# Performance work log

Measured on AMD Instinct MI355X. Metric: run time of the kernel, lower is better.

Reference implementation:

```python
import jax, jax.numpy as jnp
import numpy as np

NF, NLOC, NNEI = 4, 2048, 64
EMBED, PAIR_DIM, H = 128, 64, 8
HD = EMBED // H
EPS = 1e-5

def _ln(x, g, b):
    m = x.mean(-1, keepdims=True)
    v = ((x - m) ** 2).mean(-1, keepdims=True)
    return (x - m) * jax.lax.rsqrt(v + EPS) * g + b

def setup_inputs() -> dict:
    key = jax.random.key(0)
    ks = jax.random.split(key, 12)
    inp = {
        "query": jax.random.normal(ks[0], (NF, NLOC, EMBED), jnp.float32),
        "pair": jax.random.normal(ks[1], (NF, NLOC, NNEI, PAIR_DIM), jnp.float32),
        "nlist": jax.random.randint(ks[2], (NF, NLOC, NNEI), 0, NLOC, jnp.int64),
        "delta_pos": jax.random.normal(ks[3], (NF, NLOC, NNEI, 3), jnp.float32),
        "attn_mask": jnp.zeros((NF, H, NLOC, NNEI), jnp.float32),
        "ln_g": jnp.ones((EMBED,), jnp.float32),
        "ln_b": jnp.zeros((EMBED,), jnp.float32),
        "pn_g": jnp.ones((PAIR_DIM,), jnp.float32),
        "pn_b": jnp.zeros((PAIR_DIM,), jnp.float32),
        "Wq": jax.random.normal(ks[4], (EMBED, EMBED), jnp.float32) * (EMBED ** -0.5),
        "Wk": jax.random.normal(ks[5], (EMBED, EMBED), jnp.float32) * (EMBED ** -0.5),
        "Wv": jax.random.normal(ks[6], (EMBED, EMBED), jnp.float32) * (EMBED ** -0.5),
        "Wbias": jax.random.normal(ks[7], (H, PAIR_DIM), jnp.float32) * (PAIR_DIM ** -0.5),
        "bbias": jnp.zeros((H,), jnp.float32),
        "Wforce": jax.random.normal(ks[8], (1, EMBED), jnp.float32) * (EMBED ** -0.5),
    }
    return inp

def reference(query, pair, nlist, delta_pos, attn_mask,
              ln_g, ln_b, pn_g, pn_b, Wq, Wk, Wv, Wbias, bbias, Wforce):
    nf, nloc, _ = query.shape
    nnei = nlist.shape[-1]
    qn = _ln(query, ln_g, ln_b)            # [f,l,e]
    pn = _ln(pair, pn_g, pn_b)             # [f,l,n,p]
    scaling = HD ** -0.5
    q = (qn @ Wq.T).reshape(nf, nloc, H, HD) * scaling       # [f,l,h,d]
    k = qn @ Wk.T                                            # [f,l,e]
    v = qn @ Wv.T
    idx = nlist.reshape(nf, -1)[..., None]                   # [f,l*n,1]
    kg = jnp.take_along_axis(k, idx, axis=1).reshape(nf, nloc, nnei, H, HD)
    vg = jnp.take_along_axis(v, idx, axis=1).reshape(nf, nloc, nnei, H, HD)
    attn = jnp.einsum('flhd,flnhd->fhln', q, kg)             # [f,h,l,n]
    bias = jnp.einsum('flnp,hp->fhln', pn, Wbias) + bbias[None, :, None, None]
    probs = jax.nn.softmax(attn + attn_mask + bias, axis=-1)  # dropout off (eval)
    # rotate by delta_pos and contract with v over neighbors
    x = jnp.einsum('fhln,flnc,flnhd->flchd', probs, delta_pos, vg)
    x = x.reshape(nf, nloc, 3, EMBED)
    force = (x @ Wforce.T).squeeze(-1)                       # [f,l,3]
    return force
```

## Files before the change

kernel.cpp:

```cpp
#include <hip/hip_runtime.h>

#define NFR   4
#define NLOCC 2048
#define NNEIN 64
#define EMB   128
#define PDIM  64
#define NH    8
#define LNEPS 1e-5f
#define NROW  (NFR*NLOCC)

#define WS_Q   0
#define WS_K   (NROW*EMB)
#define WS_FV  (2*NROW*EMB)
#define WS_WVF (2*NROW*EMB + NROW*NH)
#define WS_G   (WS_WVF + NH*EMB)
#define WS_SG  (WS_G + NH*PDIM)

__device__ __forceinline__ void fma4(float4& acc, const float4 a, const float4 b) {
    acc.x = fmaf(a.x, b.x, acc.x);
    acc.y = fmaf(a.y, b.y, acc.y);
    acc.z = fmaf(a.z, b.z, acc.z);
    acc.w = fmaf(a.w, b.w, acc.w);
}
__device__ __forceinline__ void fma4s(float4& acc, const float s, const float4 b) {
    acc.x = fmaf(s, b.x, acc.x);
    acc.y = fmaf(s, b.y, acc.y);
    acc.z = fmaf(s, b.z, acc.z);
    acc.w = fmaf(s, b.w, acc.w);
}
__device__ __forceinline__ float hsum4(const float4 a) {
    return (a.x + a.y) + (a.z + a.w);
}
__device__ __forceinline__ float4 scale4(const float4 a, const float s) {
    return make_float4(a.x*s, a.y*s, a.z*s, a.w*s);
}

__global__ __launch_bounds__(256) void precompute_kernel(
    const float* __restrict__ pn_g, const float* __restrict__ pn_b,
    const float* __restrict__ Wbias, const float* __restrict__ bbias,
    const float* __restrict__ Wv, const float* __restrict__ Wforce,
    float* __restrict__ ws)
{
    const int t = threadIdx.x;
    {
        const int h  = t >> 5;
        const int e0 = (t & 31) * 4;
        float4 acc = make_float4(0.f, 0.f, 0.f, 0.f);
        #pragma unroll
        for (int d = 0; d < 16; ++d) {
            const float wf = Wforce[h*16 + d];
            const float4 wv = *(const float4*)(Wv + (size_t)(h*16 + d)*EMB + e0);
            fma4s(acc, wf, wv);
        }
        *(float4*)(ws + WS_WVF + (size_t)h*EMB + e0) = acc;
    }
    for (int idx = t; idx < NH*PDIM; idx += 256) {
        const int h = idx >> 6, p = idx & 63;
        ws[WS_G + idx] = pn_g[p] * Wbias[h*PDIM + p];
    }
    if (t < NH) {
        float sg = 0.f, c = 0.f;
        #pragma unroll 8
        for (int p = 0; p < PDIM; ++p) {
            const float wb = Wbias[t*PDIM + p];
            sg = fmaf(pn_g[p], wb, sg);
            c  = fmaf(pn_b[p], wb, c);
        }
        ws[WS_SG + t]      = sg;
        ws[WS_SG + NH + t] = c + bbias[t];
    }
}

__global__ __launch_bounds__(256, 2) void qkfv_kernel(
    const float* __restrict__ query,
    const float* __restrict__ ln_g, const float* __restrict__ ln_b,
    const float* __restrict__ Wq, const float* __restrict__ Wk,
    float* __restrict__ ws)
{
    __shared__ float gb_s[2][EMB];
    __shared__ float qn_s[16*132];
    __shared__ float wt_s[2][16*132];
    const int t = threadIdx.x;
    const int rowbase = blockIdx.x * 16;

    if (t < 64) {
        const float* src = (t < 32) ? ln_g : ln_b;
        ((float4*)gb_s[t >> 5])[t & 31] = ((const float4*)src)[t & 31];
    }

    const int r   = t >> 4;
    const int seg = t & 15;
    float4 x0 = ((const float4*)query)[(size_t)(rowbase + r)*32 + seg*2 + 0];
    float4 x1 = ((const float4*)query)[(size_t)(rowbase + r)*32 + seg*2 + 1];
    float s  = (x0.x + x0.y) + (x0.z + x0.w) + (x1.x + x1.y) + (x1.z + x1.w);
    float ss = x0.x*x0.x + x0.y*x0.y + x0.z*x0.z + x0.w*x0.w
             + x1.x*x1.x + x1.y*x1.y + x1.z*x1.z + x1.w*x1.w;
    #pragma unroll
    for (int m = 1; m < 16; m <<= 1) {
        s  += __shfl_xor(s,  m, 64);
        ss += __shfl_xor(ss, m, 64);
    }
    const float mean = s * (1.0f / 128.0f);
    const float var  = ss * (1.0f / 128.0f) - mean * mean;
    const float rstd = rsqrtf(var + LNEPS);
    __syncthreads();

    {
        const int c0 = seg * 8;
        float4 o0, o1;
        o0.x = (x0.x - mean)*rstd*gb_s[0][c0+0] + gb_s[1][c0+0];
        o0.y = (x0.y - mean)*rstd*gb_s[0][c0+1] + gb_s[1][c0+1];
        o0.z = (x0.z - mean)*rstd*gb_s[0][c0+2] + gb_s[1][c0+2];
        o0.w = (x0.w - mean)*rstd*gb_s[0][c0+3] + gb_s[1][c0+3];
        o1.x = (x1.x - mean)*rstd*gb_s[0][c0+4] + gb_s[1][c0+4];
        o1.y = (x1.y - mean)*rstd*gb_s[0][c0+5] + gb_s[1][c0+5];
        o1.z = (x1.z - mean)*rstd*gb_s[0][c0+6] + gb_s[1][c0+6];
        o1.w = (x1.w - mean)*rstd*gb_s[0][c0+7] + gb_s[1][c0+7];
        ((float4*)qn_s)[r*33 + seg*2 + 0] = o0;
        ((float4*)qn_s)[r*33 + seg*2 + 1] = o1;
    }
    __syncthreads();

    const int rp = t >> 5;
    const int r0 = rp * 2;
    const int cq = t & 31;
    const int sc0 = t >> 2;
    const int si0 = t & 3;
    const float4* qn4 = (const float4*)qn_s;

    for (int w = 0; w < 2; ++w) {
        const float4* W4 = (const float4*)((w == 0) ? Wq : Wk);
        float4 acc0 = make_float4(0.f,0.f,0.f,0.f);
        float4 acc1 = make_float4(0.f,0.f,0.f,0.f);
        {
            float4 g0 = W4[(size_t)sc0*32 + si0];
            float4 g1 = W4[(size_t)(sc0+64)*32 + si0];
            float* wt = wt_s[0];
            wt[(si0*4+0)*132 + sc0] = g0.x; wt[(si0*4+1)*132 + sc0] = g0.y;
            wt[(si0*4+2)*132 + sc0] = g0.z; wt[(si0*4+3)*132 + sc0] = g0.w;
            wt[(si0*4+0)*132 + sc0+64] = g1.x; wt[(si0*4+1)*132 + sc0+64] = g1.y;
            wt[(si0*4+2)*132 + sc0+64] = g1.z; wt[(si0*4+3)*132 + sc0+64] = g1.w;
        }
        __syncthreads();
        #pragma unroll
        for (int tau = 0; tau < 8; ++tau) {
            const int buf = tau & 1;
            float4 ng0, ng1;
            if (tau < 7) {
                ng0 = W4[(size_t)sc0*32 + (tau+1)*4 + si0];
                ng1 = W4[(size_t)(sc0+64)*32 + (tau+1)*4 + si0];
            }
            const float4* wt4 = (const float4*)wt_s[buf];
            #pragma unroll
            for (int e4 = 0; e4 < 4; ++e4) {
                float4 a0 = qn4[r0*33 + tau*4 + e4];
                float4 a1 = qn4[(r0+1)*33 + tau*4 + e4];
                const float* a0p = (const float*)&a0;
                const float* a1p = (const float*)&a1;
                #pragma unroll
                for (int ee = 0; ee < 4; ++ee) {
                    const float4 wv = wt4[(e4*4+ee)*33 + cq];
                    fma4s(acc0, a0p[ee], wv);
                    fma4s(acc1, a1p[ee], wv);
                }
            }
            if (tau < 7) {
                float* wt = wt_s[buf ^ 1];
                wt[(si0*4+0)*132 + sc0] = ng0.x; wt[(si0*4+1)*132 + sc0] = ng0.y;
                wt[(si0*4+2)*132 + sc0] = ng0.z; wt[(si0*4+3)*132 + sc0] = ng0.w;
                wt[(si0*4+0)*132 + sc0+64] = ng1.x; wt[(si0*4+1)*132 + sc0+64] = ng1.y;
                wt[(si0*4+2)*132 + sc0+64] = ng1.z; wt[(si0*4+3)*132 + sc0+64] = ng1.w;
            }
            __syncthreads();
        }
        const float sc = (w == 0) ? 0.25f : 1.0f;
        float4* dst = (float4*)(ws + (w == 0 ? WS_Q : WS_K));
        dst[(size_t)(rowbase + r0)*32 + cq]     = scale4(acc0, sc);
        dst[(size_t)(rowbase + r0 + 1)*32 + cq] = scale4(acc1, sc);
    }

    if (t < 128) {
        const int rr = t >> 3, h = t & 7;
        const float4* wvf4 = (const float4*)(ws + WS_WVF + (size_t)h*EMB);
        float4 acc = make_float4(0.f,0.f,0.f,0.f);
        #pragma unroll
        for (int ch = 0; ch < 32; ++ch)
            fma4(acc, qn4[rr*33 + ch], wvf4[ch]);
        ws[WS_FV + (size_t)(rowbase + rr)*NH + h] = hsum4(acc);
    }
}

__global__ __launch_bounds__(256, 4) void attn_force_kernel(
    const float* __restrict__ pair, const int* __restrict__ nlist,
    const float* __restrict__ delta_pos, const float* __restrict__ attn_mask,
    const float* __restrict__ ws, float* __restrict__ out)
{
    __shared__ float4 lds_k4[4*16*33];
    __shared__ float4 q_s4[32];
    __shared__ float4 G_s4[128];
    __shared__ float  csg_s[16];
    __shared__ float  logit_s[NNEIN*9];
    __shared__ float  s_s[NNEIN];
    __shared__ int    nl_s[NNEIN];

    const int t = threadIdx.x;
    const int bid = blockIdx.x;
    const int fr = bid >> 11;
    const int l  = bid & 2047;

    if (t < 16) ((int4*)nl_s)[t] = ((const int4*)(nlist + (size_t)bid*NNEIN))[t];
    __syncthreads();

    {
        const int w = t >> 6, lane = t & 63;
        const int half = lane >> 5, c = lane & 31;
        const float4* k4 = (const float4*)(ws + WS_K);
        int jj[8];
        #pragma unroll
        for (int i = 0; i < 8; ++i)
            jj[i] = nl_s[(w << 4) | (i << 1) | half];
        float4 vv[8];
        #pragma unroll
        for (int i = 0; i < 8; ++i)
            vv[i] = k4[((size_t)(fr << 11) + jj[i])*32 + c];
        #pragma unroll
        for (int i = 0; i < 8; ++i)
            lds_k4[(w*16 + ((i << 1) | half))*33 + c] = vv[i];
    }
    if (t < 32)        q_s4[t]      = ((const float4*)(ws + WS_Q + (size_t)bid*EMB))[t];
    else if (t < 160)  G_s4[t - 32] = ((const float4*)(ws + WS_G))[t - 32];
    else if (t < 164)  ((float4*)csg_s)[t - 160] = ((const float4*)(ws + WS_SG))[t - 160];
    __syncthreads();

    const int n = t >> 2, sub = t & 3;
    const int w = t >> 6;
    const int h0 = sub*2, h1 = h0 + 1;

    const float4* prow = (const float4*)(pair + ((size_t)bid*NNEIN + n)*PDIM);
    float4 pr[4];
    #pragma unroll
    for (int i = 0; i < 4; ++i) pr[i] = prow[sub*4 + i];
    float s = 0.f, ss = 0.f;
    #pragma unroll
    for (int i = 0; i < 4; ++i) {
        s  += (pr[i].x + pr[i].y) + (pr[i].z + pr[i].w);
        ss += pr[i].x*pr[i].x + pr[i].y*pr[i].y + pr[i].z*pr[i].z + pr[i].w*pr[i].w;
    }
    s  += __shfl_xor(s, 1, 64);  s  += __shfl_xor(s, 2, 64);
    ss += __shfl_xor(ss, 1, 64); ss += __shfl_xor(ss, 2, 64);
    const float mean = s * (1.0f / 64.0f);
    const float var  = ss * (1.0f / 64.0f) - mean * mean;
    const float rstd = rsqrtf(var + LNEPS);

    float d[NH];
    #pragma unroll
    for (int h = 0; h < NH; ++h) d[h] = 0.f;
    #pragma unroll
    for (int i = 0; i < 4; ++i) {
        const float* xp = (const float*)&pr[i];
        #pragma unroll
        for (int h = 0; h < NH; ++h) {
            const float4 g4 = G_s4[h*16 + sub*4 + i];
            d[h] = fmaf(xp[0], g4.x, d[h]);
            d[h] = fmaf(xp[1], g4.y, d[h]);
            d[h] = fmaf(xp[2], g4.z, d[h]);
            d[h] = fmaf(xp[3], g4.w, d[h]);
        }
    }
    #pragma unroll
    for (int h = 0; h < NH; ++h) {
        d[h] += __shfl_xor(d[h], 1, 64);
        d[h] += __shfl_xor(d[h], 2, 64);
    }

    {
        const int rbase = (w*16 + (n & 15))*33 + 8*sub;
        float4 accA = make_float4(0.f,0.f,0.f,0.f);
        float4 accB = make_float4(0.f,0.f,0.f,0.f);
        #pragma unroll
        for (int j4 = 0; j4 < 4; ++j4) {
            fma4(accA, lds_k4[rbase + j4],     q_s4[8*sub + j4]);
            fma4(accB, lds_k4[rbase + 4 + j4], q_s4[8*sub + 4 + j4]);
        }
        const float m0 = attn_mask[((size_t)(fr*NH + h0)*NLOCC + l)*NNEIN + n];
        const float m1 = attn_mask[((size_t)(fr*NH + h1)*NLOCC + l)*NNEIN + n];
        logit_s[n*9 + h0] = hsum4(accA) + rstd*(d[h0] - mean*csg_s[h0]) + csg_s[8 + h0] + m0;
        logit_s[n*9 + h1] = hsum4(accB) + rstd*(d[h1] - mean*csg_s[h1]) + csg_s[8 + h1] + m1;
    }
    __syncthreads();

    {
        const int h = t >> 5, i = t & 31;
        float a = logit_s[i*9 + h], b = logit_s[(i + 32)*9 + h];
        float m = fmaxf(a, b);
        #pragma unroll
        for (int mm = 16; mm >= 1; mm >>= 1) m = fmaxf(m, __shfl_xor(m, mm, 64));
        float ea = __expf(a - m), eb = __expf(b - m);
        float sum = ea + eb;
        #pragma unroll
        for (int mm = 16; mm >= 1; mm >>= 1) sum += __shfl_xor(sum, mm, 64);
        const float inv = 1.0f / sum;
        logit_s[i*9 + h]        = ea * inv;
        logit_s[(i + 32)*9 + h] = eb * inv;
    }
    __syncthreads();

    {
        const int j = nl_s[n];
        const float2 fv = ((const float2*)(ws + WS_FV + ((size_t)(fr << 11) + j)*NH))[sub];
        float sn = logit_s[n*9 + h0]*fv.x + logit_s[n*9 + h1]*fv.y;
        sn += __shfl_xor(sn, 1, 64);
        sn += __shfl_xor(sn, 2, 64);
        if (sub == 0) s_s[n] = sn;
    }
    __syncthreads();

    if (t < 64) {
        const float sv = s_s[t];
        const float* dp = delta_pos + ((size_t)bid*NNEIN + t)*3;
        float f0 = sv*dp[0], f1 = sv*dp[1], f2 = sv*dp[2];
        #pragma unroll
        for (int mm = 32; mm >= 1; mm >>= 1) {
            f0 += __shfl_xor(f0, mm, 64);
            f1 += __shfl_xor(f1, mm, 64);
            f2 += __shfl_xor(f2, mm, 64);
        }
        if (t == 0) {
            out[(size_t)bid*3 + 0] = f0;
            out[(size_t)bid*3 + 1] = f1;
            out[(size_t)bid*3 + 2] = f2;
        }
    }
}

extern "C" void kernel_launch(void* const* d_in, const int* in_sizes, int n_in,
                              void* d_out, int out_size, void* d_ws, size_t ws_size,
                              hipStream_t stream) {
    const float* query     = (const float*)d_in[0];
    const float* pair      = (const float*)d_in[1];
    const int*   nlist     = (const int*)d_in[2];
    const float* delta_pos = (const float*)d_in[3];
    const float* attn_mask = (const float*)d_in[4];
    const float* ln_g      = (const float*)d_in[5];
    const float* ln_b      = (const float*)d_in[6];
    const float* pn_g      = (const float*)d_in[7];
    const float* pn_b      = (const float*)d_in[8];
    const float* Wq        = (const float*)d_in[9];
    const float* Wk        = (const float*)d_in[10];
    const float* Wv        = (const float*)d_in[11];
    const float* Wbias     = (const float*)d_in[12];
    const float* bbias     = (const float*)d_in[13];
    const float* Wforce    = (const float*)d_in[14];
    float* out = (float*)d_out;
    float* ws  = (float*)d_ws;

    precompute_kernel<<<1, 256, 0, stream>>>(pn_g, pn_b, Wbias, bbias, Wv, Wforce, ws);
    qkfv_kernel<<<512, 256, 0, stream>>>(query, ln_g, ln_b, Wq, Wk, ws);
    attn_force_kernel<<<NROW, 256, 0, stream>>>(pair, nlist, delta_pos, attn_mask, ws, out);
}
```

Before: 277.6 us.

## Restructure attention kernel: register K dots, prefetch loads, fewer barriers

```diff
diff --git a/kernel.cpp b/kernel.cpp
--- a/kernel.cpp
+++ b/kernel.cpp
@@ -30,6 +30,9 @@
 }
 __device__ __forceinline__ float hsum4(const float4 a) {
     return (a.x + a.y) + (a.z + a.w);
+}
+__device__ __forceinline__ float dot4(const float4 a, const float4 b) {
+    return fmaf(a.x, b.x, fmaf(a.y, b.y, fmaf(a.z, b.z, a.w * b.w)));
 }
 __device__ __forceinline__ float4 scale4(const float4 a, const float s) {
     return make_float4(a.x*s, a.y*s, a.z*s, a.w*s);
@@ -195,103 +198,110 @@
     const float* __restrict__ delta_pos, const float* __restrict__ attn_mask,
     const float* __restrict__ ws, float* __restrict__ out)
 {
-    __shared__ float4 lds_k4[4*16*33];
-    __shared__ float4 q_s4[32];
+    __shared__ float  logit_s[NNEIN*9];
     __shared__ float4 G_s4[128];
-    __shared__ float  csg_s[16];
-    __shared__ float  logit_s[NNEIN*9];
-    __shared__ float  s_s[NNEIN];
-    __shared__ int    nl_s[NNEIN];
-
-    const int t = threadIdx.x;
-    const int bid = blockIdx.x;
-    const int fr = bid >> 11;
-    const int l  = bid & 2047;
-
-    if (t < 16) ((int4*)nl_s)[t] = ((const int4*)(nlist + (size_t)bid*NNEIN))[t];
-    __syncthreads();
-
-    {
-        const int w = t >> 6, lane = t & 63;
-        const int half = lane >> 5, c = lane & 31;
-        const float4* k4 = (const float4*)(ws + WS_K);
-        int jj[8];
+    __shared__ float  fpart[4][3];
+
+    const int t    = threadIdx.x;
+    const int bid  = blockIdx.x;
+    const int fr   = bid >> 11;
+    const int l    = bid & 2047;
+    const int w    = t >> 6;
+    const int lane = t & 63;
+    const int half = lane >> 5;
+    const int c    = lane & 31;
+    const int n    = (w << 4) | (lane >> 2);
+    const int sub  = lane & 3;
+    const int h0   = sub * 2, h1 = h0 + 1;
+    const int i32  = lane & 31;
+    const int hh   = (w << 1) | half;
+
+    const float4* prow = (const float4*)(pair + ((size_t)bid*NNEIN + n)*PDIM);
+    float4 pr0 = prow[sub*4+0];
+    float4 pr1 = prow[sub*4+1];
+    float4 pr2 = prow[sub*4+2];
+    float4 pr3 = prow[sub*4+3];
+
+    const int jv = nlist[(size_t)bid*NNEIN + lane];
+    const float4 q4c = ((const float4*)(ws + WS_Q))[(size_t)bid*32 + c];
+
+    const float mask0 = attn_mask[((size_t)(fr*NH + h0)*NLOCC + l)*NNEIN + n];
+    const float mask1 = attn_mask[((size_t)(fr*NH + h1)*NLOCC + l)*NNEIN + n];
+    const float sg0 = ws[WS_SG + h0],      sg1 = ws[WS_SG + h1];
+    const float cc0 = ws[WS_SG + NH + h0], cc1 = ws[WS_SG + NH + h1];
+
+    const float* dpA = delta_pos + ((size_t)bid*NNEIN + i32)*3;
+    const float* dpB = delta_pos + ((size_t)bid*NNEIN + i32 + 32)*3;
+    const float dpax = dpA[0], dpay = dpA[1], dpaz = dpA[2];
+    const float dpbx = dpB[0], dpby = dpB[1], dpbz = dpB[2];
+
+    if (t < 128) G_s4[t] = ((const float4*)(ws + WS_G))[t];
+
+    const int jA = __shfl(jv, i32, 64);
+    const int jB = __shfl(jv, i32 + 32, 64);
+    const float fvA = ws[WS_FV + ((size_t)(fr << 11) + jA)*NH + hh];
+    const float fvB = ws[WS_FV + ((size_t)(fr << 11) + jB)*NH + hh];
+
+    {
+        const float4* k4 = (const float4*)(ws + WS_K) + (size_t)(fr << 11)*32;
+        int jr[8];
         #pragma unroll
         for (int i = 0; i < 8; ++i)
-            jj[i] = nl_s[(w << 4) | (i << 1) | half];
-        float4 vv[8];
-        #pragma unroll
-        for (int i = 0; i < 8; ++i)
-            vv[i] = k4[((size_t)(fr << 11) + jj[i])*32 + c];
-        #pragma unroll
-        for (int i = 0; i < 8; ++i)
-            lds_k4[(w*16 + ((i << 1) | half))*33 + c] = vv[i];
-    }
-    if (t < 32)        q_s4[t]      = ((const float4*)(ws + WS_Q + (size_t)bid*EMB))[t];
-    else if (t < 160)  G_s4[t - 32] = ((const float4*)(ws + WS_G))[t - 32];
-    else if (t < 164)  ((float4*)csg_s)[t - 160] = ((const float4*)(ws + WS_SG))[t - 160];
-    __syncthreads();
-
-    const int n = t >> 2, sub = t & 3;
-    const int w = t >> 6;
-    const int h0 = sub*2, h1 = h0 + 1;
-
-    const float4* prow = (const float4*)(pair + ((size_t)bid*NNEIN + n)*PDIM);
-    float4 pr[4];
-    #pragma unroll
-    for (int i = 0; i < 4; ++i) pr[i] = prow[sub*4 + i];
-    float s = 0.f, ss = 0.f;
-    #pragma unroll
-    for (int i = 0; i < 4; ++i) {
-        s  += (pr[i].x + pr[i].y) + (pr[i].z + pr[i].w);
-        ss += pr[i].x*pr[i].x + pr[i].y*pr[i].y + pr[i].z*pr[i].z + pr[i].w*pr[i].w;
-    }
-    s  += __shfl_xor(s, 1, 64);  s  += __shfl_xor(s, 2, 64);
-    ss += __shfl_xor(ss, 1, 64); ss += __shfl_xor(ss, 2, 64);
-    const float mean = s * (1.0f / 64.0f);
-    const float var  = ss * (1.0f / 64.0f) - mean * mean;
-    const float rstd = rsqrtf(var + LNEPS);
-
-    float d[NH];
-    #pragma unroll
-    for (int h = 0; h < NH; ++h) d[h] = 0.f;
-    #pragma unroll
-    for (int i = 0; i < 4; ++i) {
-        const float* xp = (const float*)&pr[i];
+            jr[i] = __shfl(jv, (w << 4) | (i << 1) | half, 64);
+        float4 kkA[4], kkB[4];
+        #pragma unroll
+        for (int i = 0; i < 4; ++i) kkA[i] = k4[(size_t)jr[i]*32 + c];
+        #pragma unroll
+        for (int i = 0; i < 4; ++i) kkB[i] = k4[(size_t)jr[4+i]*32 + c];
+        float p[8];
+        #pragma unroll
+        for (int i = 0; i < 4; ++i) p[i]     = dot4(kkA[i], q4c);
+        #pragma unroll
+        for (int i = 0; i < 4; ++i) p[4 + i] = dot4(kkB[i], q4c);
+        #pragma unroll
+        for (int i = 0; i < 8; ++i) {
+            float pp = p[i];
+            pp += __shfl_xor(pp, 1, 64);
+            pp += __shfl_xor(pp, 2, 64);
+            if ((c & 3) == 0)
+                logit_s[((w << 4) | (i << 1) | half)*9 + (c >> 2)] = pp;
+        }
+    }
+    __syncthreads();
+
+    {
+        float s  = hsum4(pr0) + hsum4(pr1) + hsum4(pr2) + hsum4(pr3);
+        float ss = dot4(pr0, pr0) + dot4(pr1, pr1) + dot4(pr2, pr2) + dot4(pr3, pr3);
+        s  += __shfl_xor(s, 1, 64);  s  += __shfl_xor(s, 2, 64);
+        ss += __shfl_xor(ss, 1, 64); ss += __shfl_xor(ss, 2, 64);
+        const float mean = s * (1.0f / 64.0f);
+        const float var  = ss * (1.0f / 64.0f) - mean * mean;
+        const float rstd = rsqrtf(var + LNEPS);
+
+        float d[NH];
+        #pragma unroll
+        for (int h = 0; h < NH; ++h) d[h] = 0.f;
+        const float4 prq[4] = {pr0, pr1, pr2, pr3};
+        #pragma unroll
+        for (int q = 0; q < 4; ++q) {
+            #pragma unroll
+            for (int h = 0; h < NH; ++h)
+                d[h] += dot4(prq[q], G_s4[h*16 + sub*4 + q]);
+        }
         #pragma unroll
         for (int h = 0; h < NH; ++h) {
-            const float4 g4 = G_s4[h*16 + sub*4 + i];
-            d[h] = fmaf(xp[0], g4.x, d[h]);
-            d[h] = fmaf(xp[1], g4.y, d[h]);
-            d[h] = fmaf(xp[2], g4.z, d[h]);
-            d[h] = fmaf(xp[3], g4.w, d[h]);
-        }
-    }
-    #pragma unroll
-    for (int h = 0; h < NH; ++h) {
-        d[h] += __shfl_xor(d[h], 1, 64);
-        d[h] += __shfl_xor(d[h], 2, 64);
-    }
-
-    {
-        const int rbase = (w*16 + (n & 15))*33 + 8*sub;
-        float4 accA = make_float4(0.f,0.f,0.f,0.f);
-        float4 accB = make_float4(0.f,0.f,0.f,0.f);
-        #pragma unroll
-        for (int j4 = 0; j4 < 4; ++j4) {
-            fma4(accA, lds_k4[rbase + j4],     q_s4[8*sub + j4]);
-            fma4(accB, lds_k4[rbase + 4 + j4], q_s4[8*sub + 4 + j4]);
-        }
-        const float m0 = attn_mask[((size_t)(fr*NH + h0)*NLOCC + l)*NNEIN + n];
-        const float m1 = attn_mask[((size_t)(fr*NH + h1)*NLOCC + l)*NNEIN + n];
-        logit_s[n*9 + h0] = hsum4(accA) + rstd*(d[h0] - mean*csg_s[h0]) + csg_s[8 + h0] + m0;
-        logit_s[n*9 + h1] = hsum4(accB) + rstd*(d[h1] - mean*csg_s[h1]) + csg_s[8 + h1] + m1;
-    }
-    __syncthreads();
-
-    {
-        const int h = t >> 5, i = t & 31;
-        float a = logit_s[i*9 + h], b = logit_s[(i + 32)*9 + h];
+            d[h] += __shfl_xor(d[h], 1, 64);
+            d[h] += __shfl_xor(d[h], 2, 64);
+        }
+        const float b0 = rstd*(d[h0] - mean*sg0) + cc0 + mask0;
+        const float b1 = rstd*(d[h1] - mean*sg1) + cc1 + mask1;
+        logit_s[n*9 + h0] += b0;
+        logit_s[n*9 + h1] += b1;
+    }
+    __syncthreads();
+
+    {
+        float a = logit_s[i32*9 + hh], b = logit_s[(i32 + 32)*9 + hh];
         float m = fmaxf(a, b);
         #pragma unroll
         for (int mm = 16; mm >= 1; mm >>= 1) m = fmaxf(m, __shfl_xor(m, mm, 64));
@@ -300,37 +310,27 @@
         #pragma unroll
         for (int mm = 16; mm >= 1; mm >>= 1) sum += __shfl_xor(sum, mm, 64);
         const float inv = 1.0f / sum;
-        logit_s[i*9 + h]        = ea * inv;
-        logit_s[(i + 32)*9 + h] = eb * inv;
-    }
-    __syncthreads();
-
-    {
-        const int j = nl_s[n];
-        const float2 fv = ((const float2*)(ws + WS_FV + ((size_t)(fr << 11) + j)*NH))[sub];
-        float sn = logit_s[n*9 + h0]*fv.x + logit_s[n*9 + h1]*fv.y;
-        sn += __shfl_xor(sn, 1, 64);
-        sn += __shfl_xor(sn, 2, 64);
-        if (sub == 0) s_s[n] = sn;
-    }
-    __syncthreads();
-
-    if (t < 64) {
-        const float sv = s_s[t];
-        const float* dp = delta_pos + ((size_t)bid*NNEIN + t)*3;
-        float f0 = sv*dp[0], f1 = sv*dp[1], f2 = sv*dp[2];
-        #pragma unroll
-        for (int mm = 32; mm >= 1; mm >>= 1) {
+        float ca = ea * inv * fvA;
+        float cb = eb * inv * fvB;
+        ca += __shfl_xor(ca, 32, 64);
+        cb += __shfl_xor(cb, 32, 64);
+        float f0 = ca*dpax + cb*dpbx;
+        float f1 = ca*dpay + cb*dpby;
+        float f2 = ca*dpaz + cb*dpbz;
+        #pragma unroll
+        for (int mm = 1; mm <= 16; mm <<= 1) {
             f0 += __shfl_xor(f0, mm, 64);
             f1 += __shfl_xor(f1, mm, 64);
             f2 += __shfl_xor(f2, mm, 64);
         }
-        if (t == 0) {
-            out[(size_t)bid*3 + 0] = f0;
-            out[(size_t)bid*3 + 1] = f1;
-            out[(size_t)bid*3 + 2] = f2;
-        }
-    }
+        if (lane == 0) {
+            fpart[w][0] = f0; fpart[w][1] = f1; fpart[w][2] = f2;
+        }
+    }
+    __syncthreads();
+
+    if (t < 3)
+        out[(size_t)bid*3 + t] = fpart[0][t] + fpart[1][t] + fpart[2][t] + fpart[3][t];
 }
 
 extern "C" void kernel_launch(void* const* d_in, const int* in_sizes, int n_in,
```

Measured after the change: 265.2 us. -4.5%, faster.
